# Optimization experiments

Hardware: AMD Instinct MI355X
Metric: run time of the kernel (lower is better)

## Reference

```python
import jax, jax.numpy as jnp
import numpy as np

B, S, D, H = 2, 2048, 1024, 16
E = D // H  # per-head dim_q = dim_k = 64
LN_EPS = 1e-5


def setup_inputs() -> dict:
    key = jax.random.key(0)
    ks = jax.random.split(key, 12)
    s_in = 1.0 / np.sqrt(D)
    s_cat = 1.0 / np.sqrt(H * E)
    return {
        "q": jax.random.normal(ks[0], (B, S, D), jnp.float32),
        "k": jax.random.normal(ks[1], (B, S, D), jnp.float32),
        "v": jax.random.normal(ks[2], (B, S, D), jnp.float32),
        # stacked per-head projection weights [H, D, E] (acts as x @ W + b per head)
        "Wq": jax.random.uniform(ks[3], (H, D, E), jnp.float32, -s_in, s_in),
        "bq": jax.random.uniform(ks[4], (H, E), jnp.float32, -s_in, s_in),
        "Wk": jax.random.uniform(ks[5], (H, D, E), jnp.float32, -s_in, s_in),
        "bk": jax.random.uniform(ks[6], (H, E), jnp.float32, -s_in, s_in),
        "Wv": jax.random.uniform(ks[7], (H, D, E), jnp.float32, -s_in, s_in),
        "bv": jax.random.uniform(ks[8], (H, E), jnp.float32, -s_in, s_in),
        # output linear: [H*E, D]
        "Wo": jax.random.uniform(ks[9], (H * E, D), jnp.float32, -s_cat, s_cat),
        "bo": jax.random.uniform(ks[10], (D,), jnp.float32, -s_cat, s_cat),
        # LayerNorm affine params
        "gamma": jnp.ones((D,), jnp.float32),
        "beta": jnp.zeros((D,), jnp.float32),
    }


def _attention(q, k, v, Wq, bq, Wk, bk, Wv, bv, Wo, bo, gamma, beta):
    # per-head projections: [B,H,S,E]
    qh = jnp.einsum('bsd,hde->bhse', q, Wq) + bq[None, :, None, :]
    kh = jnp.einsum('bsd,hde->bhse', k, Wk) + bk[None, :, None, :]
    vh = jnp.einsum('bsd,hde->bhse', v, Wv) + bv[None, :, None, :]
    scale = jnp.asarray(E, qh.dtype) ** 0.5
    scores = jnp.einsum('bhse,bhte->bhst', qh, kh) / scale  # [B,H,S,S]
    attn = jax.nn.softmax(scores, axis=-1)
    ctx = jnp.einsum('bhst,bhte->bhse', attn, vh)  # [B,H,S,E]
    # concat heads -> [B,S,H*E], then output linear
    cat = ctx.transpose(0, 2, 1, 3).reshape(q.shape[0], q.shape[1], H * E)
    out = cat @ Wo + bo  # [B,S,D]
    # Residual (dropout = identity in eval) + LayerNorm
    x = q + out
    mu = jnp.mean(x, axis=-1, keepdims=True)
    var = jnp.mean((x - mu) ** 2, axis=-1, keepdims=True)
    return (x - mu) * jax.lax.rsqrt(var + LN_EPS) * gamma + beta


def reference(q, k, v, Wq, bq, Wk, bk, Wv, bv, Wo, bo, gamma, beta):
    return _attention(q, k, v, Wq, bq, Wk, bk, Wv, bv, Wo, bo, gamma, beta)
```

## Files before the change

### kernel.cpp

```cpp
#include <hip/hip_runtime.h>
#include <stdint.h>

#define B_  2
#define S_  2048
#define D_  1024
#define H_  16
#define E_  64
#define BH_ 32
#define M_  4096
#define NSPLIT 4
#define KCHUNK (S_ / NSPLIT)

typedef __bf16 bf16x8 __attribute__((ext_vector_type(8)));
typedef float  f32x4  __attribute__((ext_vector_type(4)));
typedef float  f32x16 __attribute__((ext_vector_type(16)));
typedef unsigned short u16;

#define QSCALE 0.180336880f

#define EXP2(x) __builtin_amdgcn_exp2f(x)

__device__ __forceinline__ u16 f2bf(float f) {
  uint32_t u = __builtin_bit_cast(uint32_t, f);
  u = (u + 0x7FFFu + ((u >> 16) & 1u)) >> 16;
  return (u16)u;
}

__device__ __forceinline__ uint32_t pkbf(float lo, float hi) {
  __bf16 a = (__bf16)lo, b = (__bf16)hi;
  return (uint32_t)__builtin_bit_cast(u16, a) |
         ((uint32_t)__builtin_bit_cast(u16, b) << 16);
}

__device__ __forceinline__ bf16x8 load_frag(const u16* p) {
  uint4 v = *(const uint4*)p;
  return __builtin_bit_cast(bf16x8, v);
}

__device__ __forceinline__ float bf2f(u16 u) {
  return __builtin_bit_cast(float, (uint32_t)u << 16);
}

__device__ __forceinline__ void gload16(const void* g, void* l) {
  auto gp = reinterpret_cast<const uint32_t __attribute__((address_space(1)))*>(
      reinterpret_cast<uintptr_t>(g));
  auto lp = reinterpret_cast<uint32_t __attribute__((address_space(3)))*>(
      reinterpret_cast<uintptr_t>(l));
  __builtin_amdgcn_global_load_lds(gp, lp, 16, 0, 0);
}

__global__ __launch_bounds__(256) void transpose_cvt(
    const float* __restrict__ in, u16* __restrict__ out, int R, int C)
{
  __shared__ float tile[32][33];
  const int b = blockIdx.z;
  in  += (size_t)b * R * C;
  out += (size_t)b * R * C;
  const int c0 = blockIdx.x * 32, r0 = blockIdx.y * 32;
  const int tx = threadIdx.x, ty = threadIdx.y;
#pragma unroll
  for (int j = 0; j < 32; j += 8)
    tile[ty + j][tx] = in[(size_t)(r0 + ty + j) * C + c0 + tx];
  __syncthreads();
#pragma unroll
  for (int j = 0; j < 32; j += 8)
    out[(size_t)(c0 + ty + j) * R + r0 + tx] = f2bf(tile[tx][ty + j]);
}

__global__ __launch_bounds__(256) void cvt3_bf16(
    const float* __restrict__ a, const float* __restrict__ b,
    const float* __restrict__ c, u16* __restrict__ out, int n)
{
  const float* src = blockIdx.y == 0 ? a : (blockIdx.y == 1 ? b : c);
  u16* dst = out + (size_t)blockIdx.y * n;
  int i = (blockIdx.x * 256 + threadIdx.x) * 4;
  if (i < n) {
    float4 v = *(const float4*)(src + i);
    ushort4 o;
    o.x = f2bf(v.x); o.y = f2bf(v.y); o.z = f2bf(v.z); o.w = f2bf(v.w);
    *(ushort4*)(dst + i) = o;
  }
}

template<int MODE>
__global__ __launch_bounds__(256) void gemm128(
    const u16* __restrict__ A, const u16* __restrict__ Bt,
    const float* __restrict__ b0, const float* __restrict__ b1,
    const float* __restrict__ b2, const float* __restrict__ resid,
    u16* __restrict__ outQ, u16* __restrict__ outK, u16* __restrict__ outV,
    float* __restrict__ outX)
{
  __shared__ __align__(16) u16 As[128 * 64];
  __shared__ __align__(16) u16 Bs[128 * 64];
  const int K  = D_;
  const int id = blockIdx.x;
  const int xcd = id & 7, slot = id >> 3;
  int mi_, ni_;
  if (MODE == 0) { ni_ = slot % 24; mi_ = (xcd << 2) | (slot / 24); }
  else           { ni_ = slot & 7;  mi_ = (xcd << 2) | (slot >> 3); }
  const int m0 = mi_ * 128;
  const int n0 = ni_ * 128;
  const int tid = threadIdx.x;
  const int w = tid >> 6, l = tid & 63;
  const int wr = w >> 1, wc = w & 1;
  const int ql = l & 31, h2 = l >> 5;

  const u16* Ause = A;
  const u16* Buse = Bt;
  const float* bias = b0;
  int third = 0, nloc = n0;
  if (MODE == 0) {
    third = n0 >> 10;
    nloc  = n0 & 1023;
    Ause  = A  + (size_t)third * M_ * D_;
    Buse  = Bt + (size_t)third * D_ * D_;
    bias  = third == 0 ? b0 : (third == 1 ? b1 : b2);
  }

  const int rr = l >> 3, gcc = ((l & 7) ^ (l >> 3)) * 8;
  const u16* aptr[4];
  const u16* bptr[4];
#pragma unroll
  for (int c = 0; c < 4; ++c) {
    const int chunk = w * 4 + c;
    aptr[c] = Ause + (size_t)(m0 + chunk * 8 + rr) * K + gcc;
    bptr[c] = Buse + (size_t)(nloc + chunk * 8 + rr) * K + gcc;
  }

  const int swz = ql & 7;
  f32x16 acc[2][2] = {};

  for (int k0 = 0; k0 < K; k0 += 64) {
    __syncthreads();
#pragma unroll
    for (int c = 0; c < 4; ++c) {
      const int chunk = w * 4 + c;
      gload16(aptr[c] + k0, &As[chunk * 8 * 64]);
      gload16(bptr[c] + k0, &Bs[chunk * 8 * 64]);
    }
    __syncthreads();
#pragma unroll
    for (int ks = 0; ks < 4; ++ks) {
      const int ch = ((ks * 2 + h2) ^ swz) * 8;
      bf16x8 af[2], bf[2];
#pragma unroll
      for (int mi = 0; mi < 2; ++mi)
        af[mi] = load_frag(&As[(wr * 64 + mi * 32 + ql) * 64 + ch]);
#pragma unroll
      for (int ni = 0; ni < 2; ++ni)
        bf[ni] = load_frag(&Bs[(wc * 64 + ni * 32 + ql) * 64 + ch]);
#pragma unroll
      for (int mi = 0; mi < 2; ++mi)
#pragma unroll
        for (int ni = 0; ni < 2; ++ni)
          acc[mi][ni] = __builtin_amdgcn_mfma_f32_32x32x16_bf16(
              af[mi], bf[ni], acc[mi][ni], 0, 0, 0);
    }
  }

  const int rbase = m0 + wr * 64;
  const int cbase = nloc + wc * 64;
#pragma unroll
  for (int mi = 0; mi < 2; ++mi) {
#pragma unroll
    for (int ni = 0; ni < 2; ++ni) {
      const int col = cbase + ni * 32 + ql;
      const float bv = bias[col];
      if (MODE == 0) {
        const int h = col >> 6, e = col & 63;
        if (third < 2) {
          u16* dst = third == 0 ? outQ : outK;
          const float sc = third == 0 ? QSCALE : 1.f;
#pragma unroll
          for (int r = 0; r < 16; ++r) {
            int row = rbase + mi * 32 + (r & 3) + 8 * (r >> 2) + 4 * h2;
            int bb = row >> 11, s = row & (S_ - 1);
            dst[((size_t)(bb * H_ + h) * S_ + s) * E_ + e] =
                f2bf((acc[mi][ni][r] + bv) * sc);
          }
        } else {
#pragma unroll
          for (int g = 0; g < 4; ++g) {
            int s0 = rbase + mi * 32 + ((g >> 1) << 4) + (h2 << 3) + ((g & 1) << 2);
            int bb = s0 >> 11, srel = s0 & (S_ - 1);
            ushort4 o;
            o.x = f2bf(acc[mi][ni][4 * g + 0] + bv);
            o.y = f2bf(acc[mi][ni][4 * g + 1] + bv);
            o.z = f2bf(acc[mi][ni][4 * g + 2] + bv);
            o.w = f2bf(acc[mi][ni][4 * g + 3] + bv);
            *(ushort4*)(&outV[((size_t)(bb * H_ + h) * E_ + e) * S_ + srel]) = o;
          }
        }
      } else {
#pragma unroll
        for (int r = 0; r < 16; ++r) {
          int row = rbase + mi * 32 + (r & 3) + 8 * (r >> 2) + 4 * h2;
          size_t idx = (size_t)row * D_ + col;
          outX[idx] = acc[mi][ni][r] + bv + resid[idx];
        }
      }
    }
  }
}

__global__ __launch_bounds__(256, 4) void attn_kernel(
    const u16* __restrict__ qh, const u16* __restrict__ kh,
    const u16* __restrict__ vT, u16* __restrict__ pA, u16* __restrict__ pB,
    float* __restrict__ ml)
{
  __shared__ __align__(16) u16 Ks[2][64 * 64];
  __shared__ __align__(16) u16 Vs[2][64 * 64];
  const int o = blockIdx.x;
  const int xcd = o & 7, slot = o >> 3;
  const int bh    = (xcd << 2) | (slot >> 6);
  const int rem   = slot & 63;
  const int split = rem >> 4;
  const int q0    = (rem & 15) * 128;
  const int kst = split * KCHUNK;
  const int tid = threadIdx.x;
  const int w = tid >> 6, l = tid & 63;
  const int ql = l & 31;
  const int h  = l >> 5;
  const int qg = q0 + w * 32 + ql;

  const size_t PSZ = (size_t)BH_ * S_ * E_;
  u16* po = split < 2 ? pA + (size_t)split * PSZ : pB + (size_t)(split - 2) * PSZ;

  const u16* qrow = qh + ((size_t)bh * S_ + qg) * E_;
  bf16x8 bq_[4];
#pragma unroll
  for (int es = 0; es < 4; ++es)
    bq_[es] = load_frag(qrow + es * 16 + h * 8);

  f32x16 oacc[2] = {};
  float lloc = 0.f;

  const int srow = w * 8 + (l >> 3);
  const int gch  = (l & 7) ^ (l >> 3);
  const u16* kbase = kh + (size_t)bh * S_ * E_;
  const u16* vbase = vT + (size_t)bh * E_ * S_;
  const int swz = (ql & 7);

  auto stage = [&](int buf, int t0) {
#pragma unroll
    for (int p = 0; p < 2; ++p) {
      gload16(kbase + (size_t)(t0 + p * 32 + srow) * E_ + gch * 8,
              &Ks[buf][p * 2048 + w * 512]);
      gload16(vbase + (size_t)(p * 32 + srow) * S_ + t0 + gch * 8,
              &Vs[buf][p * 2048 + w * 512]);
    }
  };

  stage(0, kst);
  int cur = 0;
  for (int t0 = kst; t0 < kst + KCHUNK; t0 += 64) {
    __syncthreads();
    if (t0 + 64 < kst + KCHUNK) stage(cur ^ 1, t0 + 64);

#pragma unroll
    for (int kt = 0; kt < 2; ++kt) {
      f32x16 sacc = {};
#pragma unroll
      for (int es = 0; es < 4; ++es) {
        bf16x8 ak = load_frag(
            &Ks[cur][(kt * 32 + ql) * 64 + (((es * 2 + h) ^ swz) * 8)]);
        sacc = __builtin_amdgcn_mfma_f32_32x32x16_bf16(ak, bq_[es], sacc, 0, 0, 0);
      }

      float ps0 = 0.f, ps1 = 0.f, ps2 = 0.f, ps3 = 0.f;
#pragma unroll
      for (int i = 0; i < 16; i += 4) {
        float p0 = EXP2(sacc[i + 0]); sacc[i + 0] = p0; ps0 += p0;
        float p1 = EXP2(sacc[i + 1]); sacc[i + 1] = p1; ps1 += p1;
        float p2 = EXP2(sacc[i + 2]); sacc[i + 2] = p2; ps2 += p2;
        float p3 = EXP2(sacc[i + 3]); sacc[i + 3] = p3; ps3 += p3;
      }
      lloc += (ps0 + ps1) + (ps2 + ps3);

#pragma unroll
      for (int c2 = 0; c2 < 2; ++c2) {
        uint4 pw;
        pw.x = pkbf(sacc[8 * c2 + 0], sacc[8 * c2 + 1]);
        pw.y = pkbf(sacc[8 * c2 + 2], sacc[8 * c2 + 3]);
        pw.z = pkbf(sacc[8 * c2 + 4], sacc[8 * c2 + 5]);
        pw.w = pkbf(sacc[8 * c2 + 6], sacc[8 * c2 + 7]);
        bf16x8 pb = __builtin_bit_cast(bf16x8, pw);
        const int vch = ((kt * 2 + c2) * 2 + h) ^ swz;
#pragma unroll
        for (int eb = 0; eb < 2; ++eb) {
          bf16x8 av = load_frag(&Vs[cur][(eb * 32 + ql) * 64 + vch * 8]);
          oacc[eb] = __builtin_amdgcn_mfma_f32_32x32x16_bf16(av, pb, oacc[eb], 0, 0, 0);
        }
      }
    }
    cur ^= 1;
  }

  float l_ = lloc + __shfl_xor(lloc, 32);
  const float inv = 1.f / l_;
  const size_t rowbase = ((size_t)bh * S_ + qg) * E_;
#pragma unroll
  for (int eb = 0; eb < 2; ++eb)
#pragma unroll
    for (int g = 0; g < 4; ++g) {
      ushort4 o2;
      o2.x = f2bf(oacc[eb][4 * g + 0] * inv);
      o2.y = f2bf(oacc[eb][4 * g + 1] * inv);
      o2.z = f2bf(oacc[eb][4 * g + 2] * inv);
      o2.w = f2bf(oacc[eb][4 * g + 3] * inv);
      *(ushort4*)(&po[rowbase + eb * 32 + g * 8 + h * 4]) = o2;
    }
  if (h == 0)
    ml[(size_t)(split * BH_ + bh) * S_ + qg] = l_;
}

__global__ __launch_bounds__(256) void combine_kernel(
    const u16* __restrict__ pA, const u16* __restrict__ pB,
    const float* __restrict__ ml, u16* __restrict__ cat)
{
  const int idx = blockIdx.x * 256 + threadIdx.x;
  const int e  = (idx & 15) * 4;
  const int s  = (idx >> 4) & (S_ - 1);
  const int bh = idx >> 15;
  const size_t row = (size_t)bh * S_ + s;
  const size_t PSZ = (size_t)BH_ * S_ * E_;

  float li[NSPLIT], W = 0.f;
#pragma unroll
  for (int i = 0; i < NSPLIT; ++i) {
    li[i] = ml[(size_t)(i * BH_ + bh) * S_ + s];
    W += li[i];
  }
  const float invW = 1.f / W;

  float acc0 = 0.f, acc1 = 0.f, acc2 = 0.f, acc3 = 0.f;
#pragma unroll
  for (int i = 0; i < NSPLIT; ++i) {
    const u16* p = i < 2 ? pA + (size_t)i * PSZ : pB + (size_t)(i - 2) * PSZ;
    ushort4 u = *(const ushort4*)(&p[row * E_ + e]);
    const float wi = li[i] * invW;
    acc0 += wi * bf2f(u.x);
    acc1 += wi * bf2f(u.y);
    acc2 += wi * bf2f(u.z);
    acc3 += wi * bf2f(u.w);
  }
  ushort4 o;
  o.x = f2bf(acc0); o.y = f2bf(acc1); o.z = f2bf(acc2); o.w = f2bf(acc3);
  *(ushort4*)(&cat[((size_t)(bh >> 4) * S_ + s) * D_ + (bh & 15) * E_ + e]) = o;
}

__global__ __launch_bounds__(256) void layernorm_kernel(
    float* __restrict__ x, const float* __restrict__ gamma,
    const float* __restrict__ beta)
{
  __shared__ float red[8];
  const int row = blockIdx.x;
  float* p = x + (size_t)row * D_;
  const int tid = threadIdx.x;
  float4 v = *(const float4*)(p + tid * 4);
  float s  = v.x + v.y + v.z + v.w;
  float sq = v.x * v.x + v.y * v.y + v.z * v.z + v.w * v.w;
#pragma unroll
  for (int d = 1; d < 64; d <<= 1) {
    s  += __shfl_xor(s, d);
    sq += __shfl_xor(sq, d);
  }
  const int w = tid >> 6, l = tid & 63;
  if (l == 0) { red[w] = s; red[4 + w] = sq; }
  __syncthreads();
  float S1 = red[0] + red[1] + red[2] + red[3];
  float S2 = red[4] + red[5] + red[6] + red[7];
  float mu  = S1 * (1.f / D_);
  float var = S2 * (1.f / D_) - mu * mu;
  float rinv = rsqrtf(var + 1e-5f);
  float4 g  = *(const float4*)(gamma + tid * 4);
  float4 bt = *(const float4*)(beta + tid * 4);
  float4 o;
  o.x = (v.x - mu) * rinv * g.x + bt.x;
  o.y = (v.y - mu) * rinv * g.y + bt.y;
  o.z = (v.z - mu) * rinv * g.z + bt.z;
  o.w = (v.w - mu) * rinv * g.w + bt.w;
  *(float4*)(p + tid * 4) = o;
}

extern "C" void kernel_launch(void* const* d_in, const int* in_sizes, int n_in,
                              void* d_out, int out_size, void* d_ws, size_t ws_size,
                              hipStream_t stream) {
  (void)in_sizes; (void)n_in; (void)out_size; (void)ws_size;
  const float* q     = (const float*)d_in[0];
  const float* k     = (const float*)d_in[1];
  const float* v     = (const float*)d_in[2];
  const float* Wq    = (const float*)d_in[3];
  const float* bq    = (const float*)d_in[4];
  const float* Wk    = (const float*)d_in[5];
  const float* bk    = (const float*)d_in[6];
  const float* Wv    = (const float*)d_in[7];
  const float* bv    = (const float*)d_in[8];
  const float* Wo    = (const float*)d_in[9];
  const float* bo    = (const float*)d_in[10];
  const float* gamma = (const float*)d_in[11];
  const float* beta  = (const float*)d_in[12];

  char* ws = (char*)d_ws;
  u16* qkv_bf = (u16*)ws;
  u16* Wt     = (u16*)(ws + 25165824);
  u16* WoT    = (u16*)(ws + 31457280);
  u16* qhb    = (u16*)(ws + 33554432);
  u16* khb    = (u16*)(ws + 41943040);
  u16* vTb    = (u16*)(ws + 50331648);
  u16* cat    = qkv_bf;
  u16*   pA  = (u16*)d_out;
  u16*   pB  = (u16*)(ws + 8388608);
  float* mlb = (float*)(ws + 25165824);
  float* x   = (float*)d_out;

  dim3 tb(32, 8);
  transpose_cvt<<<dim3(2, 32, 16), tb, 0, stream>>>(Wq, Wt,               1024, 64);
  transpose_cvt<<<dim3(2, 32, 16), tb, 0, stream>>>(Wk, Wt + 1048576,     1024, 64);
  transpose_cvt<<<dim3(2, 32, 16), tb, 0, stream>>>(Wv, Wt + 2097152,     1024, 64);
  transpose_cvt<<<dim3(32, 32, 1), tb, 0, stream>>>(Wo, WoT,              1024, 1024);
  cvt3_bf16<<<dim3(4096, 3), 256, 0, stream>>>(q, k, v, qkv_bf, M_ * D_);

  gemm128<0><<<768, 256, 0, stream>>>(qkv_bf, Wt, bq, bk, bv, nullptr,
                                      qhb, khb, vTb, nullptr);
  attn_kernel<<<2048, 256, 0, stream>>>(qhb, khb, vTb, pA, pB, mlb);
  combine_kernel<<<4096, 256, 0, stream>>>(pA, pB, mlb, cat);
  gemm128<1><<<256, 256, 0, stream>>>(cat, WoT, bo, nullptr, nullptr, q,
                                      nullptr, nullptr, nullptr, x);
  layernorm_kernel<<<4096, 256, 0, stream>>>(x, gamma, beta);
}
```

Measured before the change: 154.8 us.

## Fuse fp32-to-bf16 input conversion into QKV GEMM and merge weight transposes

Removes the separate cvt3_bf16 pass over q/k/v. The QKV projection GEMM now reads fp32 activations directly, packs them to bf16 in registers and stores them into LDS, which avoids writing and rereading a 24MB bf16 copy. The three per-head weight transposes are merged into one launch. The A-operand load becomes a synchronous register load rather than an async global-to-LDS load, so it adds register pressure and the loads wait on the barrier. It also reads twice the bytes per tile, and each tile is reread by 8 column blocks.

```diff
diff --git a/kernel.cpp b/kernel.cpp
--- a/kernel.cpp
+++ b/kernel.cpp
@@ -49,13 +49,15 @@
   __builtin_amdgcn_global_load_lds(gp, lp, 16, 0, 0);
 }
 
-__global__ __launch_bounds__(256) void transpose_cvt(
-    const float* __restrict__ in, u16* __restrict__ out, int R, int C)
+__global__ __launch_bounds__(256) void transpose_cvt3w(
+    const float* __restrict__ Wq, const float* __restrict__ Wk,
+    const float* __restrict__ Wv, u16* __restrict__ out)
 {
   __shared__ float tile[32][33];
-  const int b = blockIdx.z;
-  in  += (size_t)b * R * C;
-  out += (size_t)b * R * C;
+  const int z = blockIdx.z, sel = z >> 4, b = z & 15;
+  const float* in = (sel == 0 ? Wq : (sel == 1 ? Wk : Wv)) + (size_t)b * 65536;
+  u16* o = out + (size_t)sel * 1048576 + (size_t)b * 65536;
+  const int R = 1024, C = 64;
   const int c0 = blockIdx.x * 32, r0 = blockIdx.y * 32;
   const int tx = threadIdx.x, ty = threadIdx.y;
 #pragma unroll
@@ -64,27 +66,29 @@
   __syncthreads();
 #pragma unroll
   for (int j = 0; j < 32; j += 8)
+    o[(size_t)(c0 + ty + j) * R + r0 + tx] = f2bf(tile[tx][ty + j]);
+}
+
+__global__ __launch_bounds__(256) void transpose_cvt(
+    const float* __restrict__ in, u16* __restrict__ out, int R, int C)
+{
+  __shared__ float tile[32][33];
+  const int c0 = blockIdx.x * 32, r0 = blockIdx.y * 32;
+  const int tx = threadIdx.x, ty = threadIdx.y;
+#pragma unroll
+  for (int j = 0; j < 32; j += 8)
+    tile[ty + j][tx] = in[(size_t)(r0 + ty + j) * C + c0 + tx];
+  __syncthreads();
+#pragma unroll
+  for (int j = 0; j < 32; j += 8)
     out[(size_t)(c0 + ty + j) * R + r0 + tx] = f2bf(tile[tx][ty + j]);
-}
-
-__global__ __launch_bounds__(256) void cvt3_bf16(
-    const float* __restrict__ a, const float* __restrict__ b,
-    const float* __restrict__ c, u16* __restrict__ out, int n)
-{
-  const float* src = blockIdx.y == 0 ? a : (blockIdx.y == 1 ? b : c);
-  u16* dst = out + (size_t)blockIdx.y * n;
-  int i = (blockIdx.x * 256 + threadIdx.x) * 4;
-  if (i < n) {
-    float4 v = *(const float4*)(src + i);
-    ushort4 o;
-    o.x = f2bf(v.x); o.y = f2bf(v.y); o.z = f2bf(v.z); o.w = f2bf(v.w);
-    *(ushort4*)(dst + i) = o;
-  }
 }
 
 template<int MODE>
 __global__ __launch_bounds__(256) void gemm128(
-    const u16* __restrict__ A, const u16* __restrict__ Bt,
+    const float* __restrict__ Aq, const float* __restrict__ Ak,
+    const float* __restrict__ Av, const u16* __restrict__ Abf,
+    const u16* __restrict__ Bt,
     const float* __restrict__ b0, const float* __restrict__ b1,
     const float* __restrict__ b2, const float* __restrict__ resid,
     u16* __restrict__ outQ, u16* __restrict__ outK, u16* __restrict__ outV,
@@ -105,37 +109,59 @@
   const int wr = w >> 1, wc = w & 1;
   const int ql = l & 31, h2 = l >> 5;
 
-  const u16* Ause = A;
   const u16* Buse = Bt;
   const float* bias = b0;
+  const float* Af = nullptr;
+  const u16* Ause = Abf;
   int third = 0, nloc = n0;
   if (MODE == 0) {
     third = n0 >> 10;
     nloc  = n0 & 1023;
-    Ause  = A  + (size_t)third * M_ * D_;
+    Af    = third == 0 ? Aq : (third == 1 ? Ak : Av);
     Buse  = Bt + (size_t)third * D_ * D_;
     bias  = third == 0 ? b0 : (third == 1 ? b1 : b2);
   }
 
-  const int rr = l >> 3, gcc = ((l & 7) ^ (l >> 3)) * 8;
-  const u16* aptr[4];
-  const u16* bptr[4];
+  const int rr = l >> 3, gce = ((l & 7) ^ (l >> 3)) * 8;
+  const float* aptrf[4];
+  const u16*   aptr[4];
+  const u16*   bptr[4];
 #pragma unroll
   for (int c = 0; c < 4; ++c) {
     const int chunk = w * 4 + c;
-    aptr[c] = Ause + (size_t)(m0 + chunk * 8 + rr) * K + gcc;
-    bptr[c] = Buse + (size_t)(nloc + chunk * 8 + rr) * K + gcc;
+    if (MODE == 0)
+      aptrf[c] = Af + (size_t)(m0 + chunk * 8 + rr) * K + gce;
+    else
+      aptr[c]  = Ause + (size_t)(m0 + chunk * 8 + rr) * K + gce;
+    bptr[c] = Buse + (size_t)(nloc + chunk * 8 + rr) * K + gce;
   }
 
   const int swz = ql & 7;
   f32x16 acc[2][2] = {};
 
   for (int k0 = 0; k0 < K; k0 += 64) {
+    float4 a0[4], a1[4];
+    if (MODE == 0) {
+#pragma unroll
+      for (int c = 0; c < 4; ++c) {
+        a0[c] = *(const float4*)(aptrf[c] + k0);
+        a1[c] = *(const float4*)(aptrf[c] + k0 + 4);
+      }
+    }
     __syncthreads();
 #pragma unroll
     for (int c = 0; c < 4; ++c) {
       const int chunk = w * 4 + c;
-      gload16(aptr[c] + k0, &As[chunk * 8 * 64]);
+      if (MODE == 0) {
+        uint4 pw;
+        pw.x = pkbf(a0[c].x, a0[c].y);
+        pw.y = pkbf(a0[c].z, a0[c].w);
+        pw.z = pkbf(a1[c].x, a1[c].y);
+        pw.w = pkbf(a1[c].z, a1[c].w);
+        *(uint4*)(&As[chunk * 8 * 64 + l * 8]) = pw;
+      } else {
+        gload16(aptr[c] + k0, &As[chunk * 8 * 64]);
+      }
       gload16(bptr[c] + k0, &Bs[chunk * 8 * 64]);
     }
     __syncthreads();
@@ -402,30 +428,27 @@
   const float* beta  = (const float*)d_in[12];
 
   char* ws = (char*)d_ws;
-  u16* qkv_bf = (u16*)ws;
+  u16* cat    = (u16*)ws;
   u16* Wt     = (u16*)(ws + 25165824);
   u16* WoT    = (u16*)(ws + 31457280);
   u16* qhb    = (u16*)(ws + 33554432);
   u16* khb    = (u16*)(ws + 41943040);
   u16* vTb    = (u16*)(ws + 50331648);
-  u16* cat    = qkv_bf;
   u16*   pA  = (u16*)d_out;
   u16*   pB  = (u16*)(ws + 8388608);
   float* mlb = (float*)(ws + 25165824);
   float* x   = (float*)d_out;
 
   dim3 tb(32, 8);
-  transpose_cvt<<<dim3(2, 32, 16), tb, 0, stream>>>(Wq, Wt,               1024, 64);
-  transpose_cvt<<<dim3(2, 32, 16), tb, 0, stream>>>(Wk, Wt + 1048576,     1024, 64);
-  transpose_cvt<<<dim3(2, 32, 16), tb, 0, stream>>>(Wv, Wt + 2097152,     1024, 64);
-  transpose_cvt<<<dim3(32, 32, 1), tb, 0, stream>>>(Wo, WoT,              1024, 1024);
-  cvt3_bf16<<<dim3(4096, 3), 256, 0, stream>>>(q, k, v, qkv_bf, M_ * D_);
-
-  gemm128<0><<<768, 256, 0, stream>>>(qkv_bf, Wt, bq, bk, bv, nullptr,
+  transpose_cvt3w<<<dim3(2, 32, 48), tb, 0, stream>>>(Wq, Wk, Wv, Wt);
+  transpose_cvt<<<dim3(32, 32, 1), tb, 0, stream>>>(Wo, WoT, 1024, 1024);
+
+  gemm128<0><<<768, 256, 0, stream>>>(q, k, v, nullptr, Wt, bq, bk, bv, nullptr,
                                       qhb, khb, vTb, nullptr);
   attn_kernel<<<2048, 256, 0, stream>>>(qhb, khb, vTb, pA, pB, mlb);
   combine_kernel<<<4096, 256, 0, stream>>>(pA, pB, mlb, cat);
-  gemm128<1><<<256, 256, 0, stream>>>(cat, WoT, bo, nullptr, nullptr, q,
+  gemm128<1><<<256, 256, 0, stream>>>(nullptr, nullptr, nullptr, cat, WoT, bo,
+                                      nullptr, nullptr, q,
                                       nullptr, nullptr, nullptr, x);
   layernorm_kernel<<<4096, 256, 0, stream>>>(x, gamma, beta);
 }
```

After: 151.4 us. 2.2% less time.

## Double-buffer GEMM LDS tiles with prefetch and merge QKV weight transposes

Applied to the files above, without the earlier changes.

The bf16 GEMM now keeps two LDS buffers for the A and B tiles. It issues the global-to-LDS loads for the next K step before computing on the current one, and drops one barrier per iteration, so memory latency can overlap with MFMA work. This doubles LDS use per block to 64KB, which may lower occupancy. If the compiler waits on all outstanding vector-memory loads before the LDS reads, the overlap could be limited. Separately, the three per-head weight transpose launches are merged into one kernel indexed by blockIdx.z, cutting launch overhead.

```diff
diff --git a/kernel.cpp b/kernel.cpp
--- a/kernel.cpp
+++ b/kernel.cpp
@@ -49,13 +49,30 @@
   __builtin_amdgcn_global_load_lds(gp, lp, 16, 0, 0);
 }
 
+__global__ __launch_bounds__(256) void transpose_cvt3w(
+    const float* __restrict__ Wq, const float* __restrict__ Wk,
+    const float* __restrict__ Wv, u16* __restrict__ out)
+{
+  __shared__ float tile[32][33];
+  const int z = blockIdx.z, sel = z >> 4, b = z & 15;
+  const float* in = (sel == 0 ? Wq : (sel == 1 ? Wk : Wv)) + (size_t)b * 65536;
+  u16* o = out + (size_t)sel * 1048576 + (size_t)b * 65536;
+  const int R = 1024, C = 64;
+  const int c0 = blockIdx.x * 32, r0 = blockIdx.y * 32;
+  const int tx = threadIdx.x, ty = threadIdx.y;
+#pragma unroll
+  for (int j = 0; j < 32; j += 8)
+    tile[ty + j][tx] = in[(size_t)(r0 + ty + j) * C + c0 + tx];
+  __syncthreads();
+#pragma unroll
+  for (int j = 0; j < 32; j += 8)
+    o[(size_t)(c0 + ty + j) * R + r0 + tx] = f2bf(tile[tx][ty + j]);
+}
+
 __global__ __launch_bounds__(256) void transpose_cvt(
     const float* __restrict__ in, u16* __restrict__ out, int R, int C)
 {
   __shared__ float tile[32][33];
-  const int b = blockIdx.z;
-  in  += (size_t)b * R * C;
-  out += (size_t)b * R * C;
   const int c0 = blockIdx.x * 32, r0 = blockIdx.y * 32;
   const int tx = threadIdx.x, ty = threadIdx.y;
 #pragma unroll
@@ -90,8 +107,8 @@
     u16* __restrict__ outQ, u16* __restrict__ outK, u16* __restrict__ outV,
     float* __restrict__ outX)
 {
-  __shared__ __align__(16) u16 As[128 * 64];
-  __shared__ __align__(16) u16 Bs[128 * 64];
+  __shared__ __align__(16) u16 As[2][128 * 64];
+  __shared__ __align__(16) u16 Bs[2][128 * 64];
   const int K  = D_;
   const int id = blockIdx.x;
   const int xcd = id & 7, slot = id >> 3;
@@ -117,38 +134,48 @@
     bias  = third == 0 ? b0 : (third == 1 ? b1 : b2);
   }
 
-  const int rr = l >> 3, gcc = ((l & 7) ^ (l >> 3)) * 8;
+  const int rr = l >> 3, gce = ((l & 7) ^ (l >> 3)) * 8;
   const u16* aptr[4];
   const u16* bptr[4];
 #pragma unroll
   for (int c = 0; c < 4; ++c) {
     const int chunk = w * 4 + c;
-    aptr[c] = Ause + (size_t)(m0 + chunk * 8 + rr) * K + gcc;
-    bptr[c] = Buse + (size_t)(nloc + chunk * 8 + rr) * K + gcc;
+    aptr[c] = Ause + (size_t)(m0 + chunk * 8 + rr) * K + gce;
+    bptr[c] = Buse + (size_t)(nloc + chunk * 8 + rr) * K + gce;
   }
 
   const int swz = ql & 7;
   f32x16 acc[2][2] = {};
 
+#pragma unroll
+  for (int c = 0; c < 4; ++c) {
+    const int chunk = w * 4 + c;
+    gload16(aptr[c], &As[0][chunk * 8 * 64]);
+    gload16(bptr[c], &Bs[0][chunk * 8 * 64]);
+  }
+
+  int cur = 0;
   for (int k0 = 0; k0 < K; k0 += 64) {
     __syncthreads();
-#pragma unroll
-    for (int c = 0; c < 4; ++c) {
-      const int chunk = w * 4 + c;
-      gload16(aptr[c] + k0, &As[chunk * 8 * 64]);
-      gload16(bptr[c] + k0, &Bs[chunk * 8 * 64]);
-    }
-    __syncthreads();
+    const int nxt = k0 + 64;
+    if (nxt < K) {
+#pragma unroll
+      for (int c = 0; c < 4; ++c) {
+        const int chunk = w * 4 + c;
+        gload16(aptr[c] + nxt, &As[cur ^ 1][chunk * 8 * 64]);
+        gload16(bptr[c] + nxt, &Bs[cur ^ 1][chunk * 8 * 64]);
+      }
+    }
 #pragma unroll
     for (int ks = 0; ks < 4; ++ks) {
       const int ch = ((ks * 2 + h2) ^ swz) * 8;
       bf16x8 af[2], bf[2];
 #pragma unroll
       for (int mi = 0; mi < 2; ++mi)
-        af[mi] = load_frag(&As[(wr * 64 + mi * 32 + ql) * 64 + ch]);
+        af[mi] = load_frag(&As[cur][(wr * 64 + mi * 32 + ql) * 64 + ch]);
 #pragma unroll
       for (int ni = 0; ni < 2; ++ni)
-        bf[ni] = load_frag(&Bs[(wc * 64 + ni * 32 + ql) * 64 + ch]);
+        bf[ni] = load_frag(&Bs[cur][(wc * 64 + ni * 32 + ql) * 64 + ch]);
 #pragma unroll
       for (int mi = 0; mi < 2; ++mi)
 #pragma unroll
@@ -156,6 +183,7 @@
           acc[mi][ni] = __builtin_amdgcn_mfma_f32_32x32x16_bf16(
               af[mi], bf[ni], acc[mi][ni], 0, 0, 0);
     }
+    cur ^= 1;
   }
 
   const int rbase = m0 + wr * 64;
@@ -415,10 +443,8 @@
   float* x   = (float*)d_out;
 
   dim3 tb(32, 8);
-  transpose_cvt<<<dim3(2, 32, 16), tb, 0, stream>>>(Wq, Wt,               1024, 64);
-  transpose_cvt<<<dim3(2, 32, 16), tb, 0, stream>>>(Wk, Wt + 1048576,     1024, 64);
-  transpose_cvt<<<dim3(2, 32, 16), tb, 0, stream>>>(Wv, Wt + 2097152,     1024, 64);
-  transpose_cvt<<<dim3(32, 32, 1), tb, 0, stream>>>(Wo, WoT,              1024, 1024);
+  transpose_cvt3w<<<dim3(2, 32, 48), tb, 0, stream>>>(Wq, Wk, Wv, Wt);
+  transpose_cvt<<<dim3(32, 32, 1), tb, 0, stream>>>(Wo, WoT, 1024, 1024);
   cvt3_bf16<<<dim3(4096, 3), 256, 0, stream>>>(q, k, v, qkv_bf, M_ * D_);
 
   gemm128<0><<<768, 256, 0, stream>>>(qkv_bf, Wt, bq, bk, bv, nullptr,
```

Result: no change. 151.8 us (median of 2 runs) (-1.9%).
